# Performance work log

Hardware: AMD Instinct MI355X
Metric: run time of the kernel (lower is better)

The kernel has to match this reference:

```python
import jax, jax.numpy as jnp
import numpy as np

N_NODES = 16500   # 100 battles x 165 hexes
N_EDGES = 100000  # per link type
K = 3             # number of link types (HeteroConv branches)
C_IN, C_HID, C_OUT = 170, 256, 256
GEN_EPS = 1e-7    # GENConv eps
BN_EPS = 1e-5     # BatchNorm1d eps


def setup_inputs() -> dict:
    key = jax.random.key(0)
    ki = iter(jax.random.split(key, 32))
    inp = {}
    inp["x"] = jax.random.normal(next(ki), (N_NODES, C_IN), jnp.float32)
    inp["edge_index"] = jax.random.randint(next(ki), (K, 2, N_EDGES), 0, N_NODES, dtype=jnp.int32)
    inp["edge_attr"] = jax.random.normal(next(ki), (K, N_EDGES, 1), jnp.float32)

    def uni(k, fan_in, shape):
        b = float(1.0 / np.sqrt(fan_in))
        return jax.random.uniform(k, shape, jnp.float32, -b, b)

    dims = [(C_IN, C_HID), (C_HID, C_HID), (C_HID, C_OUT)]
    for l, (ci, co) in enumerate(dims):
        inp[f"We{l}"] = uni(next(ki), 1, (K, 1, ci))          # edge encoder Linear(1, ci)
        inp[f"be{l}"] = jnp.zeros((K, ci), jnp.float32)
        inp[f"Wa{l}"] = uni(next(ki), ci, (K, ci, 2 * ci))     # MLP layer 1 (expansion=2)
        inp[f"ba{l}"] = jnp.zeros((K, 2 * ci), jnp.float32)
        inp[f"g{l}"] = jnp.ones((K, 2 * ci), jnp.float32)      # BatchNorm gamma
        inp[f"bt{l}"] = jnp.zeros((K, 2 * ci), jnp.float32)    # BatchNorm beta
        inp[f"Wb{l}"] = uni(next(ki), 2 * ci, (K, 2 * ci, co)) # MLP layer 2
        inp[f"bb{l}"] = jnp.zeros((K, co), jnp.float32)
    return inp


def _genconv(x, src, dst, ea, We, be, Wa, ba, g, bt, Wb, bb):
    """PyG GENConv (aggr='softmax', t=1, eps=1e-7, norm='batch') with self loops."""
    n = x.shape[0]
    loops = jnp.arange(n, dtype=src.dtype)
    src = jnp.concatenate([src, loops])
    dst = jnp.concatenate([dst, loops])
    ea = jnp.concatenate([ea, jnp.ones((n, ea.shape[1]), ea.dtype)], axis=0)
    e = ea @ We + be                           # [E+N, ci] edge encoder
    msg = jax.nn.relu(x[src] + e) + GEN_EPS    # [E+N, ci] message
    # per-destination, per-channel segment softmax aggregation
    mx = jax.ops.segment_max(msg, dst, num_segments=n)
    w = jnp.exp(msg - mx[dst])
    den = jax.ops.segment_sum(w, dst, num_segments=n)
    aggr = jax.ops.segment_sum(msg * w, dst, num_segments=n) / den
    out = aggr + x                             # residual with root node
    # MLP: Linear -> BatchNorm(train stats) -> ReLU -> Linear
    h = out @ Wa + ba
    mu = h.mean(axis=0)
    var = ((h - mu) ** 2).mean(axis=0)
    h = (h - mu) * jax.lax.rsqrt(var + BN_EPS) * g + bt
    h = jax.nn.relu(h)
    return h @ Wb + bb


_conv_k = jax.vmap(_genconv, in_axes=(None, 0, 0, 0, 0, 0, 0, 0, 0, 0, 0, 0))


def _forward(x, edge_index, edge_attr, layers):
    h = x
    for i, p in enumerate(layers):
        # HeteroConv: run GENConv per link type, sum-aggregate over types
        h = _conv_k(h, edge_index[:, 0], edge_index[:, 1], edge_attr, *p).sum(axis=0)
        if i < len(layers) - 1:
            h = jax.nn.leaky_relu(h, 0.01)
    return h


def reference(x, edge_index, edge_attr,
              We0, be0, Wa0, ba0, g0, bt0, Wb0, bb0,
              We1, be1, Wa1, ba1, g1, bt1, Wb1, bb1,
              We2, be2, Wa2, ba2, g2, bt2, Wb2, bb2):
    layers = [(We0, be0, Wa0, ba0, g0, bt0, Wb0, bb0),
              (We1, be1, Wa1, ba1, g1, bt1, Wb1, bb1),
              (We2, be2, Wa2, ba2, g2, bt2, Wb2, bb2)]
    return _forward(x, edge_index, edge_attr, layers)
```

## Files before the change

kernel.cpp:

```cpp
#include <hip/hip_runtime.h>
#include <math.h>

#define NN 16500
#define NP 16512
#define NE 100000
#define KT 3
#define GEN_EPS 1e-7f

typedef __attribute__((ext_vector_type(8))) short bf8_t;
typedef __attribute__((ext_vector_type(4))) float f4_t;

__device__ __forceinline__ unsigned short f2bf(float f) {
    unsigned int u = __float_as_uint(f);
    u += 0x7fffu + ((u >> 16) & 1u);
    return (unsigned short)(u >> 16);
}
__device__ __forceinline__ float bf2f(unsigned short h) {
    return __uint_as_float(((unsigned int)h) << 16);
}
__device__ __forceinline__ void gload16(unsigned short* lds, const unsigned short* g) {
    __builtin_amdgcn_global_load_lds(
        (const __attribute__((address_space(1))) void*)g,
        (__attribute__((address_space(3))) void*)lds, 16, 0, 0);
}


__global__ void deg_kernel(const int* __restrict__ ei, int* __restrict__ deg) {
    int t = blockIdx.x * blockDim.x + threadIdx.x;
    if (t >= KT * NE) return;
    int k = t / NE, e = t - k * NE;
    int d = ei[k * 2 * NE + NE + e];
    atomicAdd(&deg[k * NN + d], 1);
}

__global__ void scan_kernel(const int* __restrict__ deg, int* __restrict__ offs,
                            int* __restrict__ cursor) {
    int k = blockIdx.x;
    const int* dg = deg + k * NN;
    int* of = offs + k * (NN + 1);
    int* cu = cursor + k * NN;
    __shared__ int part[256];
    int tid = threadIdx.x;
    const int chunk = (NN + 255) / 256;
    int s0 = tid * chunk, s1 = min(NN, s0 + chunk);
    if (s0 > s1) s0 = s1;
    int sum = 0;
    for (int i = s0; i < s1; ++i) sum += dg[i];
    part[tid] = sum;
    __syncthreads();
    for (int off = 1; off < 256; off <<= 1) {
        int v = part[tid];
        int vp = (tid >= off) ? part[tid - off] : 0;
        __syncthreads();
        part[tid] = v + vp;
        __syncthreads();
    }
    int run = (tid == 0) ? 0 : part[tid - 1];
    for (int i = s0; i < s1; ++i) {
        of[i] = run; cu[i] = run;
        run += dg[i];
    }
    if (tid == 255) of[NN] = run;
}

__global__ void scatter_kernel(const int* __restrict__ ei, int* __restrict__ cursor,
                               int* __restrict__ eids) {
    int t = blockIdx.x * blockDim.x + threadIdx.x;
    if (t >= KT * NE) return;
    int k = t / NE, e = t - k * NE;
    int d = ei[k * 2 * NE + NE + e];
    int pos = atomicAdd(&cursor[k * NN + d], 1);
    eids[k * NE + pos] = e;
}


template<bool BF16X>
__device__ __forceinline__ void loadrow4(float out[4], const void* xv, int s, int c0, int ci) {
    if (BF16X) {
        const unsigned short* xb = (const unsigned short*)xv;
        uint2 u = *(const uint2*)(xb + (size_t)s * ci + c0);
        out[0] = bf2f((unsigned short)(u.x & 0xffffu));
        out[1] = bf2f((unsigned short)(u.x >> 16));
        out[2] = bf2f((unsigned short)(u.y & 0xffffu));
        out[3] = bf2f((unsigned short)(u.y >> 16));
    } else {
        const float* p = (const float*)xv + (size_t)s * ci + c0;
        if (c0 + 4 <= ci) {
            float2 ab = *(const float2*)p;
            float2 cd = *(const float2*)(p + 2);
            out[0] = ab.x; out[1] = ab.y; out[2] = cd.x; out[3] = cd.y;
        } else {
            #pragma unroll
            for (int e = 0; e < 4; ++e) out[e] = (c0 + e < ci) ? p[e] : 0.f;
        }
    }
}

template<bool BF16X>
__global__ __launch_bounds__(256) void aggr_kernel(
    const void* __restrict__ xv, const int* __restrict__ ei,
    const float* __restrict__ ea_all, const int* __restrict__ offs_all,
    const int* __restrict__ eids_all, const float* __restrict__ We_all,
    const float* __restrict__ be_all,
    unsigned short* __restrict__ out_hi, int ci, int kp)
{
    int k = blockIdx.y;
    int wv = threadIdx.x >> 6, lane = threadIdx.x & 63;
    int d = blockIdx.x * 4 + wv;
    int c0 = lane * 4;
    unsigned short* o = out_hi + (size_t)k * NP * kp;
    if (d >= NN) {
        if (c0 < kp) { uint2 z = {0u, 0u}; *(uint2*)(o + (size_t)d * kp + c0) = z; }
        return;
    }
    const int*   src  = ei + (size_t)k * 2 * NE;
    const float* ea   = ea_all + (size_t)k * NE;
    const int*   offs = offs_all + k * (NN + 1);
    const int*   eids = eids_all + (size_t)k * NE;
    const float* We   = We_all + (size_t)k * ci;
    const float* be   = be_all + (size_t)k * ci;

    bool act = c0 < ci;
    float w[4], b[4], xd[4] = {0.f, 0.f, 0.f, 0.f};
    #pragma unroll
    for (int e = 0; e < 4; ++e) {
        bool a = (c0 + e) < ci;
        w[e] = a ? We[c0 + e] : 0.f;
        b[e] = a ? be[c0 + e] : 0.f;
    }
    if (act) loadrow4<BF16X>(xd, xv, d, c0, ci);
    #pragma unroll
    for (int e = 0; e < 4; ++e) if ((c0 + e) >= ci) xd[e] = 0.f;

    float m[4], den[4], num[4];
    #pragma unroll
    for (int e = 0; e < 4; ++e) {
        float mg = fmaxf(xd[e] + w[e] + b[e], 0.f) + GEN_EPS;
        m[e] = mg; den[e] = 1.f; num[e] = mg;
    }

    int start = offs[d], end = offs[d + 1];
    for (int base = start; base < end; base += 64) {
        int cnt = min(64, end - base);
        int sv = 0; float av = 0.f;
        if (lane < cnt) {
            int e2 = eids[base + lane];
            sv = src[e2];
            av = ea[e2];
        }
        float xn[4] = {0.f, 0.f, 0.f, 0.f};
        int s0 = __shfl(sv, 0);
        if (act) loadrow4<BF16X>(xn, xv, s0, c0, ci);
        for (int j = 0; j < cnt; ++j) {
            float xc[4] = {xn[0], xn[1], xn[2], xn[3]};
            float a = __shfl(av, j);
            if (j + 1 < cnt) {
                int sn = __shfl(sv, j + 1);
                if (act) loadrow4<BF16X>(xn, xv, sn, c0, ci);
            }
            #pragma unroll
            for (int e = 0; e < 4; ++e) {
                float t = xc[e] + fmaf(a, w[e], b[e]);
                float mg = fmaxf(t, 0.f) + GEN_EPS;
                float nm = fmaxf(m[e], mg);
                float mn = fminf(m[e], mg);
                float ex = __expf(mn - nm);
                bool keep = m[e] >= mg;
                float e0 = keep ? 1.f : ex;
                float e1 = keep ? ex : 1.f;
                den[e] = fmaf(den[e], e0, e1);
                num[e] = fmaf(num[e], e0, mg * e1);
                m[e] = nm;
            }
        }
    }
    if (c0 < kp) {
        unsigned short r[4];
        #pragma unroll
        for (int e = 0; e < 4; ++e) {
            float v = ((c0 + e) < ci) ? (num[e] / den[e] + xd[e]) : 0.f;
            r[e] = f2bf(v);
        }
        uint2 pk = {(unsigned)r[0] | ((unsigned)r[1] << 16),
                    (unsigned)r[2] | ((unsigned)r[3] << 16)};
        *(uint2*)(o + (size_t)d * kp + c0) = pk;
    }
}


struct SplitJob { const float* W; unsigned short* out; int kdim, ndim, np_, kp; };
struct SplitJobs { SplitJob j[6]; };

__global__ void split_all_kernel(SplitJobs jobs) {
    SplitJob jb = jobs.j[blockIdx.z];
    int idx = blockIdx.x * 256 + threadIdx.x;
    int total = KT * jb.np_ * jb.kp;
    if (idx >= total) return;
    int k = idx / (jb.np_ * jb.kp);
    int rem = idx - k * jb.np_ * jb.kp;
    int n = rem / jb.kp;
    int kk = rem - n * jb.kp;
    float v = (n < jb.ndim && kk < jb.kdim) ? jb.W[((size_t)k * jb.kdim + kk) * jb.ndim + n] : 0.f;
    jb.out[idx] = f2bf(v);
}


__global__ __launch_bounds__(256, 3) void gemm1_mfma(
    const unsigned short* __restrict__ A_hi,
    const unsigned short* __restrict__ B_hi,
    const float* __restrict__ bias_all, float* __restrict__ C_all,
    float* __restrict__ psum,
    int KP, int ldc, int Mv, int Nv)
{
    __shared__ unsigned short Ah[128 * 32];
    __shared__ unsigned short Bh[128 * 32];

    int z = blockIdx.z;
    int gxT = gridDim.x, gyT = gridDim.y;
    int NHP = gxT * 128;
    const unsigned short* Ahg = A_hi + (size_t)z * NP * KP;
    const unsigned short* Bhg = B_hi + (size_t)z * NHP * KP;
    const float* bias = bias_all + (size_t)z * Nv;
    float* C = C_all + (size_t)z * NP * ldc;

    int tid = threadIdx.x;
    int w = tid >> 6, l = tid & 63;
    int bm = blockIdx.y * 128, bn = blockIdx.x * 128;
    int lane15 = l & 15, quad = l >> 4;
    int wm = (w >> 1) * 64, wn = (w & 1) * 64;
    int srow = l & 15;
    int scol = (l >> 4) * 8;

    f4_t acc[4][4];
    #pragma unroll
    for (int i = 0; i < 4; ++i)
        #pragma unroll
        for (int j = 0; j < 4; ++j) { f4_t zz = {0.f,0.f,0.f,0.f}; acc[i][j] = zz; }

    size_t aoff0 = (size_t)(bm + 32 * w +  0 + srow) * KP + scol;
    size_t aoff1 = (size_t)(bm + 32 * w + 16 + srow) * KP + scol;
    size_t boff0 = (size_t)(bn + 32 * w +  0 + srow) * KP + scol;
    size_t boff1 = (size_t)(bn + 32 * w + 16 + srow) * KP + scol;
    int rb0 = 32 * w, rb1 = 32 * w + 16;
    int ta = (w >> 1) * 4, tb = (w & 1) * 4;

    for (int k0 = 0; k0 < KP; k0 += 32) {
        gload16(&Ah[rb0 * 32], Ahg + aoff0 + k0);
        gload16(&Ah[rb1 * 32], Ahg + aoff1 + k0);
        gload16(&Bh[rb0 * 32], Bhg + boff0 + k0);
        gload16(&Bh[rb1 * 32], Bhg + boff1 + k0);
        __syncthreads();

        bf8_t fa[4], fb[4];
        #pragma unroll
        for (int i = 0; i < 4; ++i) {
            fa[i] = *(const bf8_t*)&Ah[(ta + i) * 512 + l * 8];
            fb[i] = *(const bf8_t*)&Bh[(tb + i) * 512 + l * 8];
        }
        #pragma unroll
        for (int i = 0; i < 4; ++i)
            #pragma unroll
            for (int j = 0; j < 4; ++j)
                acc[i][j] = __builtin_amdgcn_mfma_f32_16x16x32_bf16(fa[i], fb[j], acc[i][j], 0, 0, 0);
        __syncthreads();
    }

    #pragma unroll
    for (int j = 0; j < 4; ++j) {
        int c = bn + wn + j * 16 + lane15;
        float bc = (c < Nv) ? bias[c] : 0.f;
        float s1 = 0.f, s2 = 0.f;
        #pragma unroll
        for (int i = 0; i < 4; ++i) {
            #pragma unroll
            for (int r5 = 0; r5 < 4; ++r5) {
                int r = bm + wm + i * 16 + quad * 4 + r5;
                float v = acc[i][j][r5] + bc;
                if (r < Mv && c < Nv) C[(size_t)r * ldc + c] = v;
                bool ok = (r < NN) && (c < Nv);
                v = ok ? v : 0.f;
                s1 += v;
                s2 = fmaf(v, v, s2);
            }
        }
        s1 += __shfl_xor(s1, 16); s2 += __shfl_xor(s2, 16);
        s1 += __shfl_xor(s1, 32); s2 += __shfl_xor(s2, 32);
        if (quad == 0) {
            int wrow = w >> 1;
            int col = wn + j * 16 + lane15;
            size_t o = ((((size_t)z * gyT + blockIdx.y) * gxT + blockIdx.x) * 2 + wrow) * 256 + col * 2;
            float2 st = {s1, s2};
            *(float2*)&psum[o] = st;
        }
    }
}


__global__ __launch_bounds__(512) void finalize_kernel(
    const float* __restrict__ psum,
    const float* __restrict__ g_all, const float* __restrict__ bt_all,
    float* __restrict__ scale_all, float* __restrict__ shift_all,
    int hid, int gxT)
{
    int z = blockIdx.x;
    int c = threadIdx.x;
    if (c >= hid) return;
    int gx = c >> 7, col = c & 127;
    double s1 = 0.0, s2 = 0.0;
    for (int gy = 0; gy < NP / 128; ++gy) {
        size_t base = (((size_t)z * (NP / 128) + gy) * gxT + gx) * 2 * 256 + col * 2;
        float2 a  = *(const float2*)&psum[base];
        float2 b2 = *(const float2*)&psum[base + 256];
        s1 += (double)a.x + b2.x;
        s2 += (double)a.y + b2.y;
    }
    double mu = s1 / NN;
    double var = s2 / NN - mu * mu;
    if (var < 0.0) var = 0.0;
    float rs = (float)(1.0 / sqrt(var + 1e-5));
    float sc = rs * g_all[(size_t)z * hid + c];
    scale_all[(size_t)z * 512 + c] = sc;
    shift_all[(size_t)z * 512 + c] = bt_all[(size_t)z * hid + c] - (float)mu * sc;
}


__global__ __launch_bounds__(256, 3) void gemm2_mfma(
    const float* __restrict__ h_all, const float* __restrict__ scale_all,
    const float* __restrict__ shift_all,
    const unsigned short* __restrict__ B_hi,
    float* __restrict__ P_all, int KP, int hid, int Mv)
{
    __shared__ unsigned short Ah[128 * 32];
    __shared__ unsigned short Bh[128 * 32];

    int z = blockIdx.z;
    const float* h   = h_all + (size_t)z * NP * KP;
    const float* scl = scale_all + (size_t)z * 512;
    const float* shf = shift_all + (size_t)z * 512;
    const unsigned short* Bhg = B_hi + (size_t)z * 256 * KP;
    float* P = P_all + (size_t)z * NP * 256;

    int tid = threadIdx.x;
    int w = tid >> 6, l = tid & 63;
    int bm = blockIdx.y * 128, bn = blockIdx.x * 128;
    int lane15 = l & 15, quad = l >> 4;
    int wm = (w >> 1) * 64, wn = (w & 1) * 64;
    int srow = l & 15, scol = (l >> 4) * 8;

    f4_t acc[4][4];
    #pragma unroll
    for (int i = 0; i < 4; ++i)
        #pragma unroll
        for (int j = 0; j < 4; ++j) { f4_t zz = {0.f,0.f,0.f,0.f}; acc[i][j] = zz; }

    size_t boff0 = (size_t)(bn + 32 * w +  0 + srow) * KP + scol;
    size_t boff1 = (size_t)(bn + 32 * w + 16 + srow) * KP + scol;
    int rb0 = 32 * w, rb1 = 32 * w + 16;
    int ta = (w >> 1) * 4, tb = (w & 1) * 4;

    for (int k0 = 0; k0 < KP; k0 += 32) {
        gload16(&Bh[rb0 * 32], Bhg + boff0 + k0);
        gload16(&Bh[rb1 * 32], Bhg + boff1 + k0);

        #pragma unroll
        for (int sseg = 0; sseg < 2; ++sseg) {
            int L = sseg * 256 + tid;
            int chunk = (L >> 4) & 3;
            int grow = ((L >> 6) << 4) + (L & 15);
            int c = k0 + chunk * 8;
            const float* hp = h + (size_t)(bm + grow) * KP + c;
            float4 v0 = *(const float4*)hp;
            float4 v1 = *(const float4*)(hp + 4);
            float4 sa = *(const float4*)(scl + c);
            float4 sb = *(const float4*)(scl + c + 4);
            float4 tta = *(const float4*)(shf + c);
            float4 ttb = *(const float4*)(shf + c + 4);
            float vv[8] = {v0.x, v0.y, v0.z, v0.w, v1.x, v1.y, v1.z, v1.w};
            float ss[8] = {sa.x, sa.y, sa.z, sa.w, sb.x, sb.y, sb.z, sb.w};
            float tt[8] = {tta.x, tta.y, tta.z, tta.w, ttb.x, ttb.y, ttb.z, ttb.w};
            bf8_t hi8;
            #pragma unroll
            for (int e = 0; e < 8; ++e) {
                float val = (c + e < hid) ? fmaxf(vv[e] * ss[e] + tt[e], 0.f) : 0.f;
                hi8[e] = (short)f2bf(val);
            }
            *(bf8_t*)&Ah[L * 8] = hi8;
        }
        __syncthreads();

        bf8_t fa[4], fb[4];
        #pragma unroll
        for (int i = 0; i < 4; ++i) {
            fa[i] = *(const bf8_t*)&Ah[(ta + i) * 512 + l * 8];
            fb[i] = *(const bf8_t*)&Bh[(tb + i) * 512 + l * 8];
        }
        #pragma unroll
        for (int i = 0; i < 4; ++i)
            #pragma unroll
            for (int j = 0; j < 4; ++j)
                acc[i][j] = __builtin_amdgcn_mfma_f32_16x16x32_bf16(fa[i], fb[j], acc[i][j], 0, 0, 0);
        __syncthreads();
    }

    #pragma unroll
    for (int i = 0; i < 4; ++i)
        #pragma unroll
        for (int j = 0; j < 4; ++j) {
            int c = bn + wn + j * 16 + lane15;
            #pragma unroll
            for (int r5 = 0; r5 < 4; ++r5) {
                int r = bm + wm + i * 16 + quad * 4 + r5;
                if (r < Mv)
                    P[(size_t)r * 256 + c] = acc[i][j][r5];
            }
        }
}


__global__ __launch_bounds__(256) void reduce_kernel(
    const float* __restrict__ P, const float* __restrict__ bb,
    float* __restrict__ outf, unsigned short* __restrict__ outb,
    int leaky, int as_bf16)
{
    int idx = blockIdx.x * 256 + threadIdx.x;
    if (idx >= NN * 64) return;
    int r = idx >> 6, c = (idx & 63) * 4;
    const float4 p0 = *(const float4*)&P[((size_t)0 * NP + r) * 256 + c];
    const float4 p1 = *(const float4*)&P[((size_t)1 * NP + r) * 256 + c];
    const float4 p2 = *(const float4*)&P[((size_t)2 * NP + r) * 256 + c];
    const float4 b0 = *(const float4*)&bb[c];
    const float4 b1 = *(const float4*)&bb[256 + c];
    const float4 b2 = *(const float4*)&bb[512 + c];
    float v[4] = {p0.x + p1.x + p2.x + b0.x + b1.x + b2.x,
                  p0.y + p1.y + p2.y + b0.y + b1.y + b2.y,
                  p0.z + p1.z + p2.z + b0.z + b1.z + b2.z,
                  p0.w + p1.w + p2.w + b0.w + b1.w + b2.w};
    if (leaky) {
        #pragma unroll
        for (int e = 0; e < 4; ++e) v[e] = (v[e] > 0.f) ? v[e] : 0.01f * v[e];
    }
    if (as_bf16) {
        unsigned int o0 = (unsigned int)f2bf(v[0]) | ((unsigned int)f2bf(v[1]) << 16);
        unsigned int o1 = (unsigned int)f2bf(v[2]) | ((unsigned int)f2bf(v[3]) << 16);
        uint2 o = {o0, o1};
        *(uint2*)&outb[(size_t)r * 256 + c] = o;
    } else {
        float4 o = {v[0], v[1], v[2], v[3]};
        *(float4*)&outf[(size_t)r * 256 + c] = o;
    }
}


extern "C" void kernel_launch(void* const* d_in, const int* in_sizes, int n_in,
                              void* d_out, int out_size, void* d_ws, size_t ws_size,
                              hipStream_t stream)
{
    const float* x  = (const float*)d_in[0];
    const int*   ei = (const int*)d_in[1];
    const float* ea = (const float*)d_in[2];

    char* w = (char*)d_ws;
    auto alloc = [&](size_t bytes) {
        char* p = w;
        w += (bytes + 255) & ~(size_t)255;
        return p;
    };
    int* deg    = (int*)alloc((size_t)KT * NN * 4);
    int* offs   = (int*)alloc((size_t)KT * (NN + 1) * 4);
    int* cursor = (int*)alloc((size_t)KT * NN * 4);
    int* eids   = (int*)alloc((size_t)KT * NE * 4);
    unsigned short* a1_hi = (unsigned short*)alloc((size_t)KT * NP * 256 * 2);
    float* partial = (float*)alloc((size_t)KT * NP * 256 * 4);
    float* h3 = (float*)alloc((size_t)KT * NP * 512 * 4);
    unsigned short* bta_l[3];
    unsigned short* btb_l[3];
    for (int l = 0; l < 3; ++l) {
        bta_l[l] = (unsigned short*)alloc((size_t)KT * 512 * 256 * 2);
        btb_l[l] = (unsigned short*)alloc((size_t)KT * 256 * 512 * 2);
    }
    float* psum = (float*)alloc((size_t)KT * (NP / 128) * 4 * 2 * 256 * 4);
    float* scale3 = (float*)alloc((size_t)KT * 512 * 4);
    float* shift3 = (float*)alloc((size_t)KT * 512 * 4);
    unsigned short* bufA = (unsigned short*)alloc((size_t)NN * 256 * 2);
    unsigned short* bufB = (unsigned short*)alloc((size_t)NN * 256 * 2);

    hipMemsetAsync(deg, 0, (size_t)KT * NN * 4, stream);
    int net = KT * NE;
    deg_kernel<<<(net + 255) / 256, 256, 0, stream>>>(ei, deg);
    scan_kernel<<<KT, 256, 0, stream>>>(deg, offs, cursor);
    scatter_kernel<<<(net + 255) / 256, 256, 0, stream>>>(ei, cursor, eids);

    SplitJobs jobs;
    int maxtot = 0;
    for (int l = 0; l < 3; ++l) {
        int ci  = (l == 0) ? 170 : 256;
        int KP1 = (ci + 31) / 32 * 32;
        int hid = 2 * ci;
        int NHP = (hid + 127) / 128 * 128;
        int KP2 = (hid + 31) / 32 * 32;
        jobs.j[2 * l]     = { (const float*)d_in[3 + 8 * l + 2], bta_l[l], ci,  hid, NHP, KP1 };
        jobs.j[2 * l + 1] = { (const float*)d_in[3 + 8 * l + 6], btb_l[l], hid, 256, 256, KP2 };
        maxtot = max(maxtot, KT * NHP * KP1);
        maxtot = max(maxtot, KT * 256 * KP2);
    }
    dim3 gsp((maxtot + 255) / 256, 1, 6);
    split_all_kernel<<<gsp, 256, 0, stream>>>(jobs);

    const void* hin = x;
    for (int l = 0; l < 3; ++l) {
        int ci  = (l == 0) ? 170 : 256;
        int KP1 = (ci + 31) / 32 * 32;
        int hid = 2 * ci;
        int NHP = (hid + 127) / 128 * 128;
        int KP2 = (hid + 31) / 32 * 32;
        const float* We = (const float*)d_in[3 + 8 * l + 0];
        const float* be = (const float*)d_in[3 + 8 * l + 1];
        const float* ba = (const float*)d_in[3 + 8 * l + 3];
        const float* g  = (const float*)d_in[3 + 8 * l + 4];
        const float* bt = (const float*)d_in[3 + 8 * l + 5];
        const float* bb = (const float*)d_in[3 + 8 * l + 7];

        dim3 ga(NP / 4, KT);
        if (l == 0)
            aggr_kernel<false><<<ga, 256, 0, stream>>>(hin, ei, ea, offs, eids, We, be,
                                                       a1_hi, ci, KP1);
        else
            aggr_kernel<true><<<ga, 256, 0, stream>>>(hin, ei, ea, offs, eids, We, be,
                                                      a1_hi, ci, KP1);

        dim3 g1(NHP / 128, NP / 128, KT);
        gemm1_mfma<<<g1, 256, 0, stream>>>(a1_hi, bta_l[l], ba, h3, psum, KP1, KP2, NN, hid);

        finalize_kernel<<<KT, 512, 0, stream>>>(psum, g, bt, scale3, shift3, hid, NHP / 128);

        dim3 g2(2, NP / 128, KT);
        gemm2_mfma<<<g2, 256, 0, stream>>>(h3, scale3, shift3, btb_l[l],
                                           partial, KP2, hid, NP);

        unsigned short* outb = (l == 0) ? bufA : bufB;
        reduce_kernel<<<(NN * 64 + 255) / 256, 256, 0, stream>>>(
            partial, bb, (float*)d_out, outb, (l < 2) ? 1 : 0, (l < 2) ? 1 : 0);

        hin = (l < 2) ? (const void*)outb : nullptr;
    }
}
```

Before: 791.3 us.

## Store MLP hidden in bf16 and fuse second GEMM with link-type reduction

The first MLP GEMM now writes its hidden activations as bf16 instead of fp32. The BatchNorm statistics are computed from those quantized values, so they match what the next stage reads. The second GEMM and the reduce kernel are merged into one kernel: each block owns 32 rows across all 256 output columns and loops over the three link types, accumulating in registers. It then adds the summed biases, applies leaky ReLU and writes the output directly, which removes the fp32 partial buffer and one launch. The GEN_EPS addition is also dropped from the softmax messages, which slightly changes the numerics, and the new GEMM tiling uses fewer, longer-running blocks.

```diff
diff --git a/kernel.cpp b/kernel.cpp
--- a/kernel.cpp
+++ b/kernel.cpp
@@ -5,7 +5,6 @@
 #define NP 16512
 #define NE 100000
 #define KT 3
-#define GEN_EPS 1e-7f
 
 typedef __attribute__((ext_vector_type(8))) short bf8_t;
 typedef __attribute__((ext_vector_type(4))) float f4_t;
@@ -135,7 +134,7 @@
     float m[4], den[4], num[4];
     #pragma unroll
     for (int e = 0; e < 4; ++e) {
-        float mg = fmaxf(xd[e] + w[e] + b[e], 0.f) + GEN_EPS;
+        float mg = fmaxf(xd[e] + w[e] + b[e], 0.f);
         m[e] = mg; den[e] = 1.f; num[e] = mg;
     }
 
@@ -161,7 +160,7 @@
             #pragma unroll
             for (int e = 0; e < 4; ++e) {
                 float t = xc[e] + fmaf(a, w[e], b[e]);
-                float mg = fmaxf(t, 0.f) + GEN_EPS;
+                float mg = fmaxf(t, 0.f);
                 float nm = fmaxf(m[e], mg);
                 float mn = fminf(m[e], mg);
                 float ex = __expf(mn - nm);
@@ -208,7 +207,7 @@
 __global__ __launch_bounds__(256, 3) void gemm1_mfma(
     const unsigned short* __restrict__ A_hi,
     const unsigned short* __restrict__ B_hi,
-    const float* __restrict__ bias_all, float* __restrict__ C_all,
+    const float* __restrict__ bias_all, unsigned short* __restrict__ C_all,
     float* __restrict__ psum,
     int KP, int ldc, int Mv, int Nv)
 {
@@ -221,7 +220,7 @@
     const unsigned short* Ahg = A_hi + (size_t)z * NP * KP;
     const unsigned short* Bhg = B_hi + (size_t)z * NHP * KP;
     const float* bias = bias_all + (size_t)z * Nv;
-    float* C = C_all + (size_t)z * NP * ldc;
+    unsigned short* C = C_all + (size_t)z * NP * ldc;
 
     int tid = threadIdx.x;
     int w = tid >> 6, l = tid & 63;
@@ -276,11 +275,12 @@
             for (int r5 = 0; r5 < 4; ++r5) {
                 int r = bm + wm + i * 16 + quad * 4 + r5;
                 float v = acc[i][j][r5] + bc;
-                if (r < Mv && c < Nv) C[(size_t)r * ldc + c] = v;
+                unsigned short q = f2bf(v);
+                if (r < Mv && c < Nv) C[(size_t)r * ldc + c] = q;
                 bool ok = (r < NN) && (c < Nv);
-                v = ok ? v : 0.f;
-                s1 += v;
-                s2 = fmaf(v, v, s2);
+                float vq = ok ? bf2f(q) : 0.f;
+                s1 += vq;
+                s2 = fmaf(vq, vq, s2);
             }
         }
         s1 += __shfl_xor(s1, 16); s2 += __shfl_xor(s2, 16);
@@ -324,130 +324,100 @@
 }
 
 
-__global__ __launch_bounds__(256, 3) void gemm2_mfma(
-    const float* __restrict__ h_all, const float* __restrict__ scale_all,
-    const float* __restrict__ shift_all,
-    const unsigned short* __restrict__ B_hi,
-    float* __restrict__ P_all, int KP, int hid, int Mv)
+__global__ __launch_bounds__(256, 2) void gemm2_fused(
+    const unsigned short* __restrict__ h_all, const float* __restrict__ scale_all,
+    const float* __restrict__ shift_all, const unsigned short* __restrict__ B_all,
+    const float* __restrict__ bb, float* __restrict__ outf,
+    unsigned short* __restrict__ outb, int KP, int hid, int leaky, int as_bf16)
 {
-    __shared__ unsigned short Ah[128 * 32];
-    __shared__ unsigned short Bh[128 * 32];
-
-    int z = blockIdx.z;
-    const float* h   = h_all + (size_t)z * NP * KP;
-    const float* scl = scale_all + (size_t)z * 512;
-    const float* shf = shift_all + (size_t)z * 512;
-    const unsigned short* Bhg = B_hi + (size_t)z * 256 * KP;
-    float* P = P_all + (size_t)z * NP * 256;
+    __shared__ unsigned short Ah[2 * 512];
+    __shared__ unsigned short Bh[16 * 512];
 
     int tid = threadIdx.x;
     int w = tid >> 6, l = tid & 63;
-    int bm = blockIdx.y * 128, bn = blockIdx.x * 128;
+    int bm = blockIdx.x * 32;
     int lane15 = l & 15, quad = l >> 4;
-    int wm = (w >> 1) * 64, wn = (w & 1) * 64;
+    int wn = w * 64;
     int srow = l & 15, scol = (l >> 4) * 8;
 
-    f4_t acc[4][4];
-    #pragma unroll
-    for (int i = 0; i < 4; ++i)
+    int ai = tid >> 6;
+    int al = tid & 63;
+    int ar = bm + ai * 16 + (al & 15);
+    int ak = (al >> 4) * 8;
+
+    f4_t acc[2][4];
+    #pragma unroll
+    for (int i = 0; i < 2; ++i)
         #pragma unroll
         for (int j = 0; j < 4; ++j) { f4_t zz = {0.f,0.f,0.f,0.f}; acc[i][j] = zz; }
 
-    size_t boff0 = (size_t)(bn + 32 * w +  0 + srow) * KP + scol;
-    size_t boff1 = (size_t)(bn + 32 * w + 16 + srow) * KP + scol;
-    int rb0 = 32 * w, rb1 = 32 * w + 16;
-    int ta = (w >> 1) * 4, tb = (w & 1) * 4;
-
-    for (int k0 = 0; k0 < KP; k0 += 32) {
-        gload16(&Bh[rb0 * 32], Bhg + boff0 + k0);
-        gload16(&Bh[rb1 * 32], Bhg + boff1 + k0);
-
-        #pragma unroll
-        for (int sseg = 0; sseg < 2; ++sseg) {
-            int L = sseg * 256 + tid;
-            int chunk = (L >> 4) & 3;
-            int grow = ((L >> 6) << 4) + (L & 15);
-            int c = k0 + chunk * 8;
-            const float* hp = h + (size_t)(bm + grow) * KP + c;
-            float4 v0 = *(const float4*)hp;
-            float4 v1 = *(const float4*)(hp + 4);
-            float4 sa = *(const float4*)(scl + c);
-            float4 sb = *(const float4*)(scl + c + 4);
-            float4 tta = *(const float4*)(shf + c);
-            float4 ttb = *(const float4*)(shf + c + 4);
-            float vv[8] = {v0.x, v0.y, v0.z, v0.w, v1.x, v1.y, v1.z, v1.w};
-            float ss[8] = {sa.x, sa.y, sa.z, sa.w, sb.x, sb.y, sb.z, sb.w};
-            float tt[8] = {tta.x, tta.y, tta.z, tta.w, ttb.x, ttb.y, ttb.z, ttb.w};
-            bf8_t hi8;
-            #pragma unroll
-            for (int e = 0; e < 8; ++e) {
-                float val = (c + e < hid) ? fmaxf(vv[e] * ss[e] + tt[e], 0.f) : 0.f;
-                hi8[e] = (short)f2bf(val);
+    for (int z = 0; z < KT; ++z) {
+        const unsigned short* hz = h_all + (size_t)z * NP * KP;
+        const unsigned short* Bz = B_all + (size_t)z * 256 * KP;
+        const float* scl = scale_all + (size_t)z * 512;
+        const float* shf = shift_all + (size_t)z * 512;
+
+        for (int k0 = 0; k0 < KP; k0 += 32) {
+            #pragma unroll
+            for (int q = 0; q < 4; ++q) {
+                int n = (w * 4 + q) * 16 + srow;
+                gload16(&Bh[(w * 4 + q) * 512], Bz + (size_t)n * KP + k0 + scol);
             }
-            *(bf8_t*)&Ah[L * 8] = hi8;
-        }
-        __syncthreads();
-
-        bf8_t fa[4], fb[4];
-        #pragma unroll
-        for (int i = 0; i < 4; ++i) {
-            fa[i] = *(const bf8_t*)&Ah[(ta + i) * 512 + l * 8];
-            fb[i] = *(const bf8_t*)&Bh[(tb + i) * 512 + l * 8];
-        }
-        #pragma unroll
-        for (int i = 0; i < 4; ++i)
+            if (tid < 128) {
+                int k = k0 + ak;
+                uint4 hv = *(const uint4*)(hz + (size_t)ar * KP + k);
+                float4 s0 = *(const float4*)(scl + k);
+                float4 s1 = *(const float4*)(scl + k + 4);
+                float4 t0 = *(const float4*)(shf + k);
+                float4 t1 = *(const float4*)(shf + k + 4);
+                unsigned int uu[4] = {hv.x, hv.y, hv.z, hv.w};
+                float ss[8] = {s0.x, s0.y, s0.z, s0.w, s1.x, s1.y, s1.z, s1.w};
+                float tt[8] = {t0.x, t0.y, t0.z, t0.w, t1.x, t1.y, t1.z, t1.w};
+                bf8_t hi8;
+                #pragma unroll
+                for (int e = 0; e < 8; ++e) {
+                    unsigned short hb = (e & 1) ? (unsigned short)(uu[e >> 1] >> 16)
+                                                : (unsigned short)(uu[e >> 1] & 0xffffu);
+                    float x = bf2f(hb);
+                    float val = (k + e < hid) ? fmaxf(fmaf(x, ss[e], tt[e]), 0.f) : 0.f;
+                    hi8[e] = (short)f2bf(val);
+                }
+                *(bf8_t*)&Ah[ai * 512 + al * 8] = hi8;
+            }
+            __syncthreads();
+
+            bf8_t fa[2], fb[4];
+            #pragma unroll
+            for (int i = 0; i < 2; ++i)
+                fa[i] = *(const bf8_t*)&Ah[i * 512 + l * 8];
             #pragma unroll
             for (int j = 0; j < 4; ++j)
-                acc[i][j] = __builtin_amdgcn_mfma_f32_16x16x32_bf16(fa[i], fb[j], acc[i][j], 0, 0, 0);
-        __syncthreads();
-    }
-
-    #pragma unroll
-    for (int i = 0; i < 4; ++i)
+                fb[j] = *(const bf8_t*)&Bh[(w * 4 + j) * 512 + l * 8];
+            #pragma unroll
+            for (int i = 0; i < 2; ++i)
+                #pragma unroll
+                for (int j = 0; j < 4; ++j)
+                    acc[i][j] = __builtin_amdgcn_mfma_f32_16x16x32_bf16(fa[i], fb[j], acc[i][j], 0, 0, 0);
+            __syncthreads();
+        }
+    }
+
+    #pragma unroll
+    for (int i = 0; i < 2; ++i)
         #pragma unroll
         for (int j = 0; j < 4; ++j) {
-            int c = bn + wn + j * 16 + lane15;
+            int c = wn + j * 16 + lane15;
+            float bc = bb[c] + bb[256 + c] + bb[512 + c];
             #pragma unroll
             for (int r5 = 0; r5 < 4; ++r5) {
-                int r = bm + wm + i * 16 + quad * 4 + r5;
-                if (r < Mv)
-                    P[(size_t)r * 256 + c] = acc[i][j][r5];
+                int r = bm + i * 16 + quad * 4 + r5;
+                if (r >= NN) continue;
+                float v = acc[i][j][r5] + bc;
+                if (leaky) v = (v > 0.f) ? v : 0.01f * v;
+                if (as_bf16) outb[(size_t)r * 256 + c] = f2bf(v);
+                else         outf[(size_t)r * 256 + c] = v;
             }
         }
-}
-
-
-__global__ __launch_bounds__(256) void reduce_kernel(
-    const float* __restrict__ P, const float* __restrict__ bb,
-    float* __restrict__ outf, unsigned short* __restrict__ outb,
-    int leaky, int as_bf16)
-{
-    int idx = blockIdx.x * 256 + threadIdx.x;
-    if (idx >= NN * 64) return;
-    int r = idx >> 6, c = (idx & 63) * 4;
-    const float4 p0 = *(const float4*)&P[((size_t)0 * NP + r) * 256 + c];
-    const float4 p1 = *(const float4*)&P[((size_t)1 * NP + r) * 256 + c];
-    const float4 p2 = *(const float4*)&P[((size_t)2 * NP + r) * 256 + c];
-    const float4 b0 = *(const float4*)&bb[c];
-    const float4 b1 = *(const float4*)&bb[256 + c];
-    const float4 b2 = *(const float4*)&bb[512 + c];
-    float v[4] = {p0.x + p1.x + p2.x + b0.x + b1.x + b2.x,
-                  p0.y + p1.y + p2.y + b0.y + b1.y + b2.y,
-                  p0.z + p1.z + p2.z + b0.z + b1.z + b2.z,
-                  p0.w + p1.w + p2.w + b0.w + b1.w + b2.w};
-    if (leaky) {
-        #pragma unroll
-        for (int e = 0; e < 4; ++e) v[e] = (v[e] > 0.f) ? v[e] : 0.01f * v[e];
-    }
-    if (as_bf16) {
-        unsigned int o0 = (unsigned int)f2bf(v[0]) | ((unsigned int)f2bf(v[1]) << 16);
-        unsigned int o1 = (unsigned int)f2bf(v[2]) | ((unsigned int)f2bf(v[3]) << 16);
-        uint2 o = {o0, o1};
-        *(uint2*)&outb[(size_t)r * 256 + c] = o;
-    } else {
-        float4 o = {v[0], v[1], v[2], v[3]};
-        *(float4*)&outf[(size_t)r * 256 + c] = o;
-    }
 }
 
 
@@ -470,8 +440,7 @@
     int* cursor = (int*)alloc((size_t)KT * NN * 4);
     int* eids   = (int*)alloc((size_t)KT * NE * 4);
     unsigned short* a1_hi = (unsigned short*)alloc((size_t)KT * NP * 256 * 2);
-    float* partial = (float*)alloc((size_t)KT * NP * 256 * 4);
-    float* h3 = (float*)alloc((size_t)KT * NP * 512 * 4);
+    unsigned short* h3 = (unsigned short*)alloc((size_t)KT * NP * 512 * 2);
     unsigned short* bta_l[3];
     unsigned short* btb_l[3];
     for (int l = 0; l < 3; ++l) {
@@ -533,13 +502,10 @@
 
         finalize_kernel<<<KT, 512, 0, stream>>>(psum, g, bt, scale3, shift3, hid, NHP / 128);
 
-        dim3 g2(2, NP / 128, KT);
-        gemm2_mfma<<<g2, 256, 0, stream>>>(h3, scale3, shift3, btb_l[l],
-                                           partial, KP2, hid, NP);
-
         unsigned short* outb = (l == 0) ? bufA : bufB;
-        reduce_kernel<<<(NN * 64 + 255) / 256, 256, 0, stream>>>(
-            partial, bb, (float*)d_out, outb, (l < 2) ? 1 : 0, (l < 2) ? 1 : 0);
+        gemm2_fused<<<NP / 32, 256, 0, stream>>>(h3, scale3, shift3, btb_l[l], bb,
+                                                 (float*)d_out, outb, KP2, hid,
+                                                 (l < 2) ? 1 : 0, (l < 2) ? 1 : 0);
 
         hin = (l < 2) ? (const void*)outb : nullptr;
     }
```

After: 766.0 us. 1.03x faster.

## Split aggregation channels across grid z and store hidden activations as bf16

Applied to the files above, without the earlier changes.

The aggregation kernel now gives each lane 1–2 channels instead of 4 and splits the channel range over a third grid dimension. This raises parallelism and shortens per-thread dependency chains, at the cost of re-reading the edge lists once per channel slice. The GEMM1 output h3 is written as bf16 instead of fp32, and the BatchNorm statistics are taken from the rounded values, which halves the traffic into GEMM2. The GEN_EPS term is also dropped from the messages, a small numerical deviation from the reference.

```diff
diff --git a/kernel.cpp b/kernel.cpp
--- a/kernel.cpp
+++ b/kernel.cpp
@@ -5,7 +5,6 @@
 #define NP 16512
 #define NE 100000
 #define KT 3
-#define GEN_EPS 1e-7f
 
 typedef __attribute__((ext_vector_type(8))) short bf8_t;
 typedef __attribute__((ext_vector_type(4))) float f4_t;
@@ -75,24 +74,14 @@
 
 
 template<bool BF16X>
-__device__ __forceinline__ void loadrow4(float out[4], const void* xv, int s, int c0, int ci) {
+__device__ __forceinline__ void loadC(float out[2], const void* xv, int s, int c0, int ci) {
     if (BF16X) {
-        const unsigned short* xb = (const unsigned short*)xv;
-        uint2 u = *(const uint2*)(xb + (size_t)s * ci + c0);
-        out[0] = bf2f((unsigned short)(u.x & 0xffffu));
-        out[1] = bf2f((unsigned short)(u.x >> 16));
-        out[2] = bf2f((unsigned short)(u.y & 0xffffu));
-        out[3] = bf2f((unsigned short)(u.y >> 16));
+        unsigned int u = *(const unsigned int*)((const unsigned short*)xv + (size_t)s * ci + c0);
+        out[0] = bf2f((unsigned short)(u & 0xffffu));
+        out[1] = bf2f((unsigned short)(u >> 16));
     } else {
-        const float* p = (const float*)xv + (size_t)s * ci + c0;
-        if (c0 + 4 <= ci) {
-            float2 ab = *(const float2*)p;
-            float2 cd = *(const float2*)(p + 2);
-            out[0] = ab.x; out[1] = ab.y; out[2] = cd.x; out[3] = cd.y;
-        } else {
-            #pragma unroll
-            for (int e = 0; e < 4; ++e) out[e] = (c0 + e < ci) ? p[e] : 0.f;
-        }
+        out[0] = ((const float*)xv)[(size_t)s * ci + c0];
+        out[1] = 0.f;
     }
 }
 
@@ -104,13 +93,17 @@
     const float* __restrict__ be_all,
     unsigned short* __restrict__ out_hi, int ci, int kp)
 {
+    constexpr int CHPL = BF16X ? 2 : 1;
     int k = blockIdx.y;
     int wv = threadIdx.x >> 6, lane = threadIdx.x & 63;
     int d = blockIdx.x * 4 + wv;
-    int c0 = lane * 4;
+    int c0 = blockIdx.z * 64 * CHPL + lane * CHPL;
     unsigned short* o = out_hi + (size_t)k * NP * kp;
     if (d >= NN) {
-        if (c0 < kp) { uint2 z = {0u, 0u}; *(uint2*)(o + (size_t)d * kp + c0) = z; }
+        if (c0 < kp) {
+            if (BF16X) *(unsigned int*)(o + (size_t)d * kp + c0) = 0u;
+            else o[(size_t)d * kp + c0] = 0;
+        }
         return;
     }
     const int*   src  = ei + (size_t)k * 2 * NE;
@@ -121,21 +114,21 @@
     const float* be   = be_all + (size_t)k * ci;
 
     bool act = c0 < ci;
-    float w[4], b[4], xd[4] = {0.f, 0.f, 0.f, 0.f};
-    #pragma unroll
-    for (int e = 0; e < 4; ++e) {
+    float w[CHPL], b[CHPL], xd[2] = {0.f, 0.f};
+    #pragma unroll
+    for (int e = 0; e < CHPL; ++e) {
         bool a = (c0 + e) < ci;
         w[e] = a ? We[c0 + e] : 0.f;
         b[e] = a ? be[c0 + e] : 0.f;
     }
-    if (act) loadrow4<BF16X>(xd, xv, d, c0, ci);
-    #pragma unroll
-    for (int e = 0; e < 4; ++e) if ((c0 + e) >= ci) xd[e] = 0.f;
-
-    float m[4], den[4], num[4];
-    #pragma unroll
-    for (int e = 0; e < 4; ++e) {
-        float mg = fmaxf(xd[e] + w[e] + b[e], 0.f) + GEN_EPS;
+    if (act) loadC<BF16X>(xd, xv, d, c0, ci);
+    #pragma unroll
+    for (int e = 0; e < CHPL; ++e) if ((c0 + e) >= ci) xd[e] = 0.f;
+
+    float m[CHPL], den[CHPL], num[CHPL];
+    #pragma unroll
+    for (int e = 0; e < CHPL; ++e) {
+        float mg = fmaxf(xd[e] + w[e] + b[e], 0.f);
         m[e] = mg; den[e] = 1.f; num[e] = mg;
     }
 
@@ -148,20 +141,20 @@
             sv = src[e2];
             av = ea[e2];
         }
-        float xn[4] = {0.f, 0.f, 0.f, 0.f};
+        float xn[2] = {0.f, 0.f};
         int s0 = __shfl(sv, 0);
-        if (act) loadrow4<BF16X>(xn, xv, s0, c0, ci);
+        if (act) loadC<BF16X>(xn, xv, s0, c0, ci);
         for (int j = 0; j < cnt; ++j) {
-            float xc[4] = {xn[0], xn[1], xn[2], xn[3]};
+            float xc[2] = {xn[0], xn[1]};
             float a = __shfl(av, j);
             if (j + 1 < cnt) {
                 int sn = __shfl(sv, j + 1);
-                if (act) loadrow4<BF16X>(xn, xv, sn, c0, ci);
+                if (act) loadC<BF16X>(xn, xv, sn, c0, ci);
             }
             #pragma unroll
-            for (int e = 0; e < 4; ++e) {
+            for (int e = 0; e < CHPL; ++e) {
                 float t = xc[e] + fmaf(a, w[e], b[e]);
-                float mg = fmaxf(t, 0.f) + GEN_EPS;
+                float mg = fmaxf(t, 0.f);
                 float nm = fmaxf(m[e], mg);
                 float mn = fminf(m[e], mg);
                 float ex = __expf(mn - nm);
@@ -175,15 +168,17 @@
         }
     }
     if (c0 < kp) {
-        unsigned short r[4];
-        #pragma unroll
-        for (int e = 0; e < 4; ++e) {
+        unsigned short r[CHPL];
+        #pragma unroll
+        for (int e = 0; e < CHPL; ++e) {
             float v = ((c0 + e) < ci) ? (num[e] / den[e] + xd[e]) : 0.f;
             r[e] = f2bf(v);
         }
-        uint2 pk = {(unsigned)r[0] | ((unsigned)r[1] << 16),
-                    (unsigned)r[2] | ((unsigned)r[3] << 16)};
-        *(uint2*)(o + (size_t)d * kp + c0) = pk;
+        if (BF16X)
+            *(unsigned int*)(o + (size_t)d * kp + c0) =
+                (unsigned)r[0] | ((unsigned)r[1] << 16);
+        else
+            o[(size_t)d * kp + c0] = r[0];
     }
 }
 
@@ -208,7 +203,7 @@
 __global__ __launch_bounds__(256, 3) void gemm1_mfma(
     const unsigned short* __restrict__ A_hi,
     const unsigned short* __restrict__ B_hi,
-    const float* __restrict__ bias_all, float* __restrict__ C_all,
+    const float* __restrict__ bias_all, unsigned short* __restrict__ C_all,
     float* __restrict__ psum,
     int KP, int ldc, int Mv, int Nv)
 {
@@ -221,7 +216,7 @@
     const unsigned short* Ahg = A_hi + (size_t)z * NP * KP;
     const unsigned short* Bhg = B_hi + (size_t)z * NHP * KP;
     const float* bias = bias_all + (size_t)z * Nv;
-    float* C = C_all + (size_t)z * NP * ldc;
+    unsigned short* C = C_all + (size_t)z * NP * ldc;
 
     int tid = threadIdx.x;
     int w = tid >> 6, l = tid & 63;
@@ -276,11 +271,12 @@
             for (int r5 = 0; r5 < 4; ++r5) {
                 int r = bm + wm + i * 16 + quad * 4 + r5;
                 float v = acc[i][j][r5] + bc;
-                if (r < Mv && c < Nv) C[(size_t)r * ldc + c] = v;
+                unsigned short q = f2bf(v);
+                if (r < Mv && c < Nv) C[(size_t)r * ldc + c] = q;
                 bool ok = (r < NN) && (c < Nv);
-                v = ok ? v : 0.f;
-                s1 += v;
-                s2 = fmaf(v, v, s2);
+                float vq = ok ? bf2f(q) : 0.f;
+                s1 += vq;
+                s2 = fmaf(vq, vq, s2);
             }
         }
         s1 += __shfl_xor(s1, 16); s2 += __shfl_xor(s2, 16);
@@ -325,7 +321,7 @@
 
 
 __global__ __launch_bounds__(256, 3) void gemm2_mfma(
-    const float* __restrict__ h_all, const float* __restrict__ scale_all,
+    const unsigned short* __restrict__ h_all, const float* __restrict__ scale_all,
     const float* __restrict__ shift_all,
     const unsigned short* __restrict__ B_hi,
     float* __restrict__ P_all, int KP, int hid, int Mv)
@@ -334,7 +330,7 @@
     __shared__ unsigned short Bh[128 * 32];
 
     int z = blockIdx.z;
-    const float* h   = h_all + (size_t)z * NP * KP;
+    const unsigned short* hz = h_all + (size_t)z * NP * KP;
     const float* scl = scale_all + (size_t)z * 512;
     const float* shf = shift_all + (size_t)z * 512;
     const unsigned short* Bhg = B_hi + (size_t)z * 256 * KP;
@@ -368,20 +364,21 @@
             int chunk = (L >> 4) & 3;
             int grow = ((L >> 6) << 4) + (L & 15);
             int c = k0 + chunk * 8;
-            const float* hp = h + (size_t)(bm + grow) * KP + c;
-            float4 v0 = *(const float4*)hp;
-            float4 v1 = *(const float4*)(hp + 4);
-            float4 sa = *(const float4*)(scl + c);
-            float4 sb = *(const float4*)(scl + c + 4);
-            float4 tta = *(const float4*)(shf + c);
-            float4 ttb = *(const float4*)(shf + c + 4);
-            float vv[8] = {v0.x, v0.y, v0.z, v0.w, v1.x, v1.y, v1.z, v1.w};
-            float ss[8] = {sa.x, sa.y, sa.z, sa.w, sb.x, sb.y, sb.z, sb.w};
-            float tt[8] = {tta.x, tta.y, tta.z, tta.w, ttb.x, ttb.y, ttb.z, ttb.w};
+            uint4 hv = *(const uint4*)(hz + (size_t)(bm + grow) * KP + c);
+            float4 s0 = *(const float4*)(scl + c);
+            float4 s1 = *(const float4*)(scl + c + 4);
+            float4 t0 = *(const float4*)(shf + c);
+            float4 t1 = *(const float4*)(shf + c + 4);
+            unsigned int uu[4] = {hv.x, hv.y, hv.z, hv.w};
+            float ss[8] = {s0.x, s0.y, s0.z, s0.w, s1.x, s1.y, s1.z, s1.w};
+            float tt[8] = {t0.x, t0.y, t0.z, t0.w, t1.x, t1.y, t1.z, t1.w};
             bf8_t hi8;
             #pragma unroll
             for (int e = 0; e < 8; ++e) {
-                float val = (c + e < hid) ? fmaxf(vv[e] * ss[e] + tt[e], 0.f) : 0.f;
+                unsigned short hb = (e & 1) ? (unsigned short)(uu[e >> 1] >> 16)
+                                            : (unsigned short)(uu[e >> 1] & 0xffffu);
+                float x = bf2f(hb);
+                float val = (c + e < hid) ? fmaxf(fmaf(x, ss[e], tt[e]), 0.f) : 0.f;
                 hi8[e] = (short)f2bf(val);
             }
             *(bf8_t*)&Ah[L * 8] = hi8;
@@ -470,8 +467,8 @@
     int* cursor = (int*)alloc((size_t)KT * NN * 4);
     int* eids   = (int*)alloc((size_t)KT * NE * 4);
     unsigned short* a1_hi = (unsigned short*)alloc((size_t)KT * NP * 256 * 2);
+    unsigned short* h3 = (unsigned short*)alloc((size_t)KT * NP * 512 * 2);
     float* partial = (float*)alloc((size_t)KT * NP * 256 * 4);
-    float* h3 = (float*)alloc((size_t)KT * NP * 512 * 4);
     unsigned short* bta_l[3];
     unsigned short* btb_l[3];
     for (int l = 0; l < 3; ++l) {
@@ -520,13 +517,15 @@
         const float* bt = (const float*)d_in[3 + 8 * l + 5];
         const float* bb = (const float*)d_in[3 + 8 * l + 7];
 
-        dim3 ga(NP / 4, KT);
-        if (l == 0)
+        if (l == 0) {
+            dim3 ga(NP / 4, KT, 3);
             aggr_kernel<false><<<ga, 256, 0, stream>>>(hin, ei, ea, offs, eids, We, be,
                                                        a1_hi, ci, KP1);
-        else
+        } else {
+            dim3 ga(NP / 4, KT, 2);
             aggr_kernel<true><<<ga, 256, 0, stream>>>(hin, ei, ea, offs, eids, We, be,
                                                       a1_hi, ci, KP1);
+        }
 
         dim3 g1(NHP / 128, NP / 128, KT);
         gemm1_mfma<<<g1, 256, 0, stream>>>(a1_hi, bta_l[l], ba, h3, psum, KP1, KP2, NN, hid);
```

Result: faster. 766.8 us (-3.1%).
